# Optimization experiments

Measured on AMD Instinct MI355X. Metric: run time of the kernel, lower is better.

The kernel has to match this reference:

```python
import jax, jax.numpy as jnp
import numpy as np

EPS = 1e-12  # torch F.normalize eps

def setup_inputs() -> dict:
    key = jax.random.key(0)
    k1, k2, k3, k4 = jax.random.split(key, 4)
    B, S, T, D, r = 8, 50, 77, 1024, 16
    h = jax.random.normal(k1, (B, S, T, D), dtype=jnp.float32)
    # R init: randn / sqrt(D), matching the torch module
    R = jax.random.normal(k2, (S, r, D), dtype=jnp.float32) / np.sqrt(D).astype(np.float32)
    # W, b are zero-init in the module; use small random values so the edit is non-trivial
    W = jax.random.normal(k3, (S, r, D), dtype=jnp.float32) * 0.02
    b = jax.random.normal(k4, (S, r), dtype=jnp.float32) * 0.02
    return {"h": h, "R": R, "W": W, "b": b}

def reference(h, R, W, b):
    # h: (B, S, T, D); R, W: (S, r, D); b: (S, r)
    # Per step t: Phi(h_t) = h_t + Rn_t^T (W_t h_t + b_t - Rn_t h_t), Rn = row-normalized R
    norm = jnp.sqrt(jnp.sum(R * R, axis=-1, keepdims=True))
    Rn = R / jnp.maximum(norm, EPS)
    Rh = jnp.einsum('bstd,srd->bstr', h, Rn)
    Wh = jnp.einsum('bstd,srd->bstr', h, W) + b[None, :, None, :]
    delta = jnp.einsum('bstr,srd->bstd', Wh - Rh, Rn)
    return h + delta
```

## Files before the change

kernel.cpp:

```cpp
#include <hip/hip_runtime.h>


typedef __attribute__((ext_vector_type(8))) short short8;
typedef __attribute__((ext_vector_type(4))) float floatx4;

__device__ __forceinline__ short f2bf(float f) {
  unsigned u = __float_as_uint(f);
  u += 0x7fffu + ((u >> 16) & 1u);
  return (short)(u >> 16);
}

#define S_ 50
#define T_ 77
#define NTOK 616

__global__ __launch_bounds__(256) void loreft_prep(
    const float* __restrict__ RG, const float* __restrict__ WG,
    short* __restrict__ Mg, short* __restrict__ Rg) {
  __shared__ float RnL[16][1024];
  const int s = blockIdx.x;
  const int tid = threadIdx.x;
  const int lane = tid & 63;
  const int wvi = tid >> 6;

#pragma unroll
  for (int rr = 0; rr < 4; ++rr) {
    const int r = wvi * 4 + rr;
    const floatx4* Rrow = (const floatx4*)(RG + (size_t)((s * 16 + r) << 10));
    const floatx4* Wrow = (const floatx4*)(WG + (size_t)((s * 16 + r) << 10));
    floatx4 rv0 = Rrow[lane * 4 + 0];
    floatx4 rv1 = Rrow[lane * 4 + 1];
    floatx4 rv2 = Rrow[lane * 4 + 2];
    floatx4 rv3 = Rrow[lane * 4 + 3];
    float ss = 0.f;
#pragma unroll
    for (int j = 0; j < 4; ++j)
      ss += rv0[j] * rv0[j] + rv1[j] * rv1[j] + rv2[j] * rv2[j] + rv3[j] * rv3[j];
#pragma unroll
    for (int m = 1; m < 64; m <<= 1) ss += __shfl_xor(ss, m);
    const float inv = 1.0f / fmaxf(sqrtf(ss), 1e-12f);

    floatx4 wa0 = Wrow[lane * 4 + 0];
    floatx4 wa1 = Wrow[lane * 4 + 1];
    floatx4 wa2 = Wrow[lane * 4 + 2];
    floatx4 wa3 = Wrow[lane * 4 + 3];
    float rn[16];
    short8 m0, m1;
#pragma unroll
    for (int j = 0; j < 4; ++j) {
      rn[j]      = rv0[j] * inv;  m0[j]     = f2bf(wa0[j] - rn[j]);
      rn[4 + j]  = rv1[j] * inv;  m0[4 + j] = f2bf(wa1[j] - rn[4 + j]);
      rn[8 + j]  = rv2[j] * inv;  m1[j]     = f2bf(wa2[j] - rn[8 + j]);
      rn[12 + j] = rv3[j] * inv;  m1[4 + j] = f2bf(wa3[j] - rn[12 + j]);
    }
    short* mdst = Mg + (size_t)(s * 16 + r) * 1024 + lane * 16;
    *(short8*)mdst = m0;
    *(short8*)(mdst + 8) = m1;
#pragma unroll
    for (int jj = 0; jj < 16; ++jj) RnL[r][lane * 16 + jj] = rn[jj];
  }
  __syncthreads();

#pragma unroll
  for (int dd = 0; dd < 4; ++dd) {
    const int d = dd * 256 + tid;
    short8 lo8, hi8;
#pragma unroll
    for (int rj = 0; rj < 8; ++rj) {
      lo8[rj] = f2bf(RnL[rj][d]);
      hi8[rj] = f2bf(RnL[rj + 8][d]);
    }
    short* dst = Rg + ((size_t)s * 1024 + d) * 16;
    *(short8*)dst = lo8;
    *(short8*)(dst + 8) = hi8;
  }
}

__global__ __launch_bounds__(256, 2) void loreft_main(
    const float* __restrict__ hG, const float* __restrict__ bG,
    const short* __restrict__ Mg, const short* __restrict__ Rg,
    float* __restrict__ outG) {
  __shared__ float hT[16 * 1024];

  const int tid = threadIdx.x;
  const int lane = tid & 63;
  const int wvi = tid >> 6;
  const int m16 = lane & 15;
  const int quad = lane >> 4;
  const int tile = blockIdx.x;
  const int s = blockIdx.y;
  const int tokbase = tile * 16;

#pragma unroll
  for (int rr = 0; rr < 4; ++rr) {
    const int rloc = wvi * 4 + rr;
    int tok = tokbase + rloc; if (tok > NTOK - 1) tok = NTOK - 1;
    const int bb = tok / T_;
    const int tt = tok - bb * T_;
    const float* rsrc = hG + (((size_t)((bb * S_ + s) * T_ + tt)) << 10);
    const int rsw = rloc & 7;
    const int lsw = lane ^ rsw;
#pragma unroll
    for (int g = 0; g < 4; ++g) {
      const float* gsrc = rsrc + ((g * 64 + lsw) << 2);
      __builtin_amdgcn_global_load_lds(
          (const __attribute__((address_space(1))) void*)gsrc,
          (__attribute__((address_space(3))) void*)&hT[rloc * 1024 + g * 256],
          16, 0, 0);
    }
  }

  int tokA = tokbase + m16; if (tokA > NTOK - 1) tokA = NTOK - 1;
  const int bb1 = tokA / T_;
  const int tt1 = tokA - bb1 * T_;
  const size_t rowoff = ((size_t)((bb1 * S_ + s) * T_ + tt1)) << 10;
  const short* mrow = Mg + (size_t)(s * 16 + m16) * 1024 + quad * 8;
  const float bias = bG[s * 16 + m16];
  const int sw = m16 & 7;
  const float* hls = &hT[m16 * 1024];

  __syncthreads();

  floatx4 acc = {0.f, 0.f, 0.f, 0.f};
#pragma unroll
  for (int kg = 0; kg < 4; ++kg) {
    short8 mf[8];
#pragma unroll
    for (int j = 0; j < 8; ++j)
      mf[j] = *(const short8*)(mrow + (kg * 8 + j) * 32);
#pragma unroll
    for (int j = 0; j < 8; ++j) {
      const int kb = kg * 8 + j;
      const int blk = kb * 8 + quad * 2;
      floatx4 p0 = *(const floatx4*)(hls + (((blk) ^ sw) << 2));
      floatx4 p1 = *(const floatx4*)(hls + (((blk + 1) ^ sw) << 2));
      short8 af;
#pragma unroll
      for (int i = 0; i < 4; ++i) { af[i] = f2bf(p0[i]); af[4 + i] = f2bf(p1[i]); }
      acc = __builtin_amdgcn_mfma_f32_16x16x32_bf16(af, mf[j], acc, 0, 0, 0);
    }
  }

  float cf[4];
#pragma unroll
  for (int i = 0; i < 4; ++i) cf[i] = acc[i] + bias;

  unsigned lo = ((unsigned)(unsigned short)f2bf(cf[0])) |
                (((unsigned)(unsigned short)f2bf(cf[1])) << 16);
  unsigned hi = ((unsigned)(unsigned short)f2bf(cf[2])) |
                (((unsigned)(unsigned short)f2bf(cf[3])) << 16);
  short8 bfrag;
  {
    const int srcbase = ((m16 >> 2) << 4) + ((quad & 1) << 3);
    const int regsel = m16 & 3;
#pragma unroll
    for (int j = 0; j < 8; ++j) {
      unsigned vlo = __shfl(lo, srcbase + j);
      unsigned vhi = __shfl(hi, srcbase + j);
      unsigned v32 = (regsel & 2) ? vhi : vlo;
      bfrag[j] = (short)((regsel & 1) ? (v32 >> 16) : (v32 & 0xffffu));
    }
  }
  const short8 zero8 = {0, 0, 0, 0, 0, 0, 0, 0};
  if (quad >= 2) bfrag = zero8;

  float* orow = outG + rowoff;
  const bool valE = (tokbase + m16) < NTOK;
  const int q16 = (quad & 1) << 3;
  const short* rbase = Rg + (size_t)s * (1024 * 16) + q16;
  const int dt0 = wvi * 16;

  short8 ar[4];
#pragma unroll
  for (int j = 0; j < 4; ++j) {
    const int dt = dt0 + j;
    ar[j] = (quad < 2) ? *(const short8*)(rbase + (dt * 16 + m16) * 16) : zero8;
  }
#pragma unroll
  for (int g = 0; g < 4; ++g) {
    short8 nr[4];
    if (g < 3) {
#pragma unroll
      for (int j = 0; j < 4; ++j) {
        const int dt = dt0 + (g + 1) * 4 + j;
        nr[j] = (quad < 2) ? *(const short8*)(rbase + (dt * 16 + m16) * 16) : zero8;
      }
    }
#pragma unroll
    for (int j = 0; j < 4; ++j) {
      const int dt = dt0 + g * 4 + j;
      floatx4 z = {0.f, 0.f, 0.f, 0.f};
      floatx4 dv = __builtin_amdgcn_mfma_f32_16x16x32_bf16(ar[j], bfrag, z, 0, 0, 0);
      floatx4 hv = *(const floatx4*)(&hT[m16 * 1024 + (((dt * 4 + quad) ^ sw) << 2)]);
      if (valE) {
        floatx4 o;
#pragma unroll
        for (int i = 0; i < 4; ++i) o[i] = hv[i] + dv[i];
        *(floatx4*)(orow + dt * 16 + quad * 4) = o;
      }
    }
    if (g < 3) {
#pragma unroll
      for (int j = 0; j < 4; ++j) ar[j] = nr[j];
    }
  }
}

extern "C" void kernel_launch(void* const* d_in, const int* in_sizes, int n_in,
                              void* d_out, int out_size, void* d_ws, size_t ws_size,
                              hipStream_t stream) {
  const float* h = (const float*)d_in[0];
  const float* R = (const float*)d_in[1];
  const float* W = (const float*)d_in[2];
  const float* b = (const float*)d_in[3];
  short* Mg = (short*)d_ws;
  short* Rg = Mg + (size_t)S_ * 16 * 1024;
  loreft_prep<<<dim3(S_), 256, 0, stream>>>(R, W, Mg, Rg);
  loreft_main<<<dim3(39, S_), 256, 0, stream>>>(h, b, Mg, Rg, (float*)d_out);
}
```

Before: 263.2 us.

## Stage h tile in LDS as bf16 and re-read h from global for residual

Instead of direct global-to-LDS fp32 loads, each thread loads h into registers, converts to bf16 once, and stores a swizzled bf16 tile in LDS. This halves LDS use (64KB to 32KB) so the launch bound is raised to 4 blocks per CU, and it removes the repeated per-MFMA fp32-to-bf16 conversion. The fp32 residual h is now re-read from global (probably an L2 hit) during the output phase, which adds global traffic and register pressure in exchange for occupancy.

New measurement: 269.7 us. 1.02x slower.

```diff
diff --git a/kernel.cpp b/kernel.cpp
--- a/kernel.cpp
+++ b/kernel.cpp
@@ -76,11 +76,11 @@
   }
 }
 
-__global__ __launch_bounds__(256, 2) void loreft_main(
+__global__ __launch_bounds__(256, 4) void loreft_main(
     const float* __restrict__ hG, const float* __restrict__ bG,
     const short* __restrict__ Mg, const short* __restrict__ Rg,
     float* __restrict__ outG) {
-  __shared__ float hT[16 * 1024];
+  __shared__ short hB[16 * 1024];
 
   const int tid = threadIdx.x;
   const int lane = tid & 63;
@@ -91,33 +91,42 @@
   const int s = blockIdx.y;
   const int tokbase = tile * 16;
 
-#pragma unroll
-  for (int rr = 0; rr < 4; ++rr) {
-    const int rloc = wvi * 4 + rr;
-    int tok = tokbase + rloc; if (tok > NTOK - 1) tok = NTOK - 1;
+  floatx4 st[16];
+#pragma unroll
+  for (int it = 0; it < 8; ++it) {
+    const int e = it * 2048 + tid * 8;
+    const int row = e >> 10;
+    const int col = e & 1023;
+    int tok = tokbase + row; if (tok > NTOK - 1) tok = NTOK - 1;
     const int bb = tok / T_;
     const int tt = tok - bb * T_;
-    const float* rsrc = hG + (((size_t)((bb * S_ + s) * T_ + tt)) << 10);
-    const int rsw = rloc & 7;
-    const int lsw = lane ^ rsw;
-#pragma unroll
-    for (int g = 0; g < 4; ++g) {
-      const float* gsrc = rsrc + ((g * 64 + lsw) << 2);
-      __builtin_amdgcn_global_load_lds(
-          (const __attribute__((address_space(1))) void*)gsrc,
-          (__attribute__((address_space(3))) void*)&hT[rloc * 1024 + g * 256],
-          16, 0, 0);
-    }
+    const float* src = hG + (((size_t)((bb * S_ + s) * T_ + tt)) << 10) + col;
+    st[2 * it]     = *(const floatx4*)(src);
+    st[2 * it + 1] = *(const floatx4*)(src + 4);
+  }
+#pragma unroll
+  for (int it = 0; it < 8; ++it) {
+    short8 v;
+#pragma unroll
+    for (int i = 0; i < 4; ++i) {
+      v[i]     = f2bf(st[2 * it][i]);
+      v[4 + i] = f2bf(st[2 * it + 1][i]);
+    }
+    const int e = it * 2048 + tid * 8;
+    const int row = e >> 10;
+    const int b = (e & 1023) >> 3;
+    *(short8*)(hB + row * 1024 + ((b ^ (row & 7)) << 3)) = v;
   }
 
   int tokA = tokbase + m16; if (tokA > NTOK - 1) tokA = NTOK - 1;
   const int bb1 = tokA / T_;
   const int tt1 = tokA - bb1 * T_;
   const size_t rowoff = ((size_t)((bb1 * S_ + s) * T_ + tt1)) << 10;
+  const float* hrow = hG + rowoff;
   const short* mrow = Mg + (size_t)(s * 16 + m16) * 1024 + quad * 8;
   const float bias = bG[s * 16 + m16];
   const int sw = m16 & 7;
-  const float* hls = &hT[m16 * 1024];
+  const short* hls = hB + m16 * 1024;
 
   __syncthreads();
 
@@ -131,12 +140,7 @@
 #pragma unroll
     for (int j = 0; j < 8; ++j) {
       const int kb = kg * 8 + j;
-      const int blk = kb * 8 + quad * 2;
-      floatx4 p0 = *(const floatx4*)(hls + (((blk) ^ sw) << 2));
-      floatx4 p1 = *(const floatx4*)(hls + (((blk + 1) ^ sw) << 2));
-      short8 af;
-#pragma unroll
-      for (int i = 0; i < 4; ++i) { af[i] = f2bf(p0[i]); af[4 + i] = f2bf(p1[i]); }
+      short8 af = *(const short8*)(hls + (((kb * 4 + quad) ^ sw) << 3));
       acc = __builtin_amdgcn_mfma_f32_16x16x32_bf16(af, mf[j], acc, 0, 0, 0);
     }
   }
@@ -171,19 +175,23 @@
   const int dt0 = wvi * 16;
 
   short8 ar[4];
+  floatx4 hv[4];
 #pragma unroll
   for (int j = 0; j < 4; ++j) {
     const int dt = dt0 + j;
     ar[j] = (quad < 2) ? *(const short8*)(rbase + (dt * 16 + m16) * 16) : zero8;
+    hv[j] = *(const floatx4*)(hrow + dt * 16 + quad * 4);
   }
 #pragma unroll
   for (int g = 0; g < 4; ++g) {
     short8 nr[4];
+    floatx4 nh[4];
     if (g < 3) {
 #pragma unroll
       for (int j = 0; j < 4; ++j) {
         const int dt = dt0 + (g + 1) * 4 + j;
         nr[j] = (quad < 2) ? *(const short8*)(rbase + (dt * 16 + m16) * 16) : zero8;
+        nh[j] = *(const floatx4*)(hrow + dt * 16 + quad * 4);
       }
     }
 #pragma unroll
@@ -191,17 +199,16 @@
       const int dt = dt0 + g * 4 + j;
       floatx4 z = {0.f, 0.f, 0.f, 0.f};
       floatx4 dv = __builtin_amdgcn_mfma_f32_16x16x32_bf16(ar[j], bfrag, z, 0, 0, 0);
-      floatx4 hv = *(const floatx4*)(&hT[m16 * 1024 + (((dt * 4 + quad) ^ sw) << 2)]);
       if (valE) {
         floatx4 o;
 #pragma unroll
-        for (int i = 0; i < 4; ++i) o[i] = hv[i] + dv[i];
+        for (int i = 0; i < 4; ++i) o[i] = hv[j][i] + dv[i];
         *(floatx4*)(orow + dt * 16 + quad * 4) = o;
       }
     }
     if (g < 3) {
 #pragma unroll
-      for (int j = 0; j < 4; ++j) ar[j] = nr[j];
+      for (int j = 0; j < 4; ++j) { ar[j] = nr[j]; hv[j] = nh[j]; }
     }
   }
 }
```
